# Performance work log

Hardware: AMD Instinct MI355X
Metric: run time of the kernel (lower is better)

The kernel has to match this reference:

```python
import jax, jax.numpy as jnp
import numpy as np

PADDING = 1
STRIDE = 1

def setup_inputs() -> dict:
    key = jax.random.key(0)
    k1, k2 = jax.random.split(key)
    x = jax.random.normal(k1, (32, 64, 64, 64), dtype=jnp.float32)
    # kaiming_normal fan_out, relu: std = sqrt(2 / (out_ch * k * k))
    fan_out = 128 * 3 * 3
    std = np.sqrt(2.0 / fan_out).astype(np.float32)
    weight = jax.random.normal(k2, (128, 64, 3, 3), dtype=jnp.float32) * std
    bias = jnp.zeros((128,), dtype=jnp.float32)
    return {"x": x, "weight": weight, "bias": bias}

def reference(x, weight, bias):
    # Faithful to the unfold+multiply+sum path, which computes a standard
    # cross-correlation conv2d (torch conv semantics) with stride/padding.
    out = jax.lax.conv_general_dilated(
        x, weight,
        window_strides=(STRIDE, STRIDE),
        padding=[(PADDING, PADDING), (PADDING, PADDING)],
        dimension_numbers=("NCHW", "OIHW", "NCHW"),
    )
    return out + bias[None, :, None, None]
```

## Files before the change

### kernel.cpp

```cpp
#include <hip/hip_runtime.h>


typedef short short8 __attribute__((ext_vector_type(8)));
typedef float f32x4  __attribute__((ext_vector_type(4)));

static __device__ __forceinline__ unsigned short f2bf(float f) {
    unsigned int u = __float_as_uint(f);
    u = (u + 0x7FFFu + ((u >> 16) & 1u)) >> 16;
    return (unsigned short)u;
}
static __device__ __forceinline__ unsigned int pk2(float lo, float hi) {
    return (unsigned int)f2bf(lo) | ((unsigned int)f2bf(hi) << 16);
}
static __device__ __forceinline__ void gload16(const void* g, void* l) {
    __builtin_amdgcn_global_load_lds(
        (const __attribute__((address_space(1))) void*)g,
        (__attribute__((address_space(3))) void*)l, 16, 0, 0);
}

__global__ __launch_bounds__(256)
void prep_xp(const float* __restrict__ x, unsigned short* __restrict__ xP)
{
    const int hp = blockIdx.x, n = blockIdx.y, tid = threadIdx.x;
    unsigned short* rowBase = xP + (((size_t)n * 66 + hp) * 66) * 64;
    if (hp == 0 || hp == 65) {
        uint4 z; z.x = z.y = z.z = z.w = 0u;
        for (int i = tid; i < 528; i += 256) ((uint4*)rowBase)[i] = z;
        return;
    }
    __shared__ float T[64][65];
    const int h = hp - 1;
    const size_t nbase = (size_t)n * 262144 + (size_t)h * 64;
    #pragma unroll
    for (int i = 0; i < 16; ++i) {
        int idx = tid + i * 256;
        int ci = idx >> 6, w = idx & 63;
        T[ci][w] = x[nbase + (size_t)ci * 4096 + w];
    }
    __syncthreads();
    if (tid < 16) {
        uint4 z; z.x = z.y = z.z = z.w = 0u;
        int wp = (tid >> 3) * 65;
        ((uint4*)(rowBase + wp * 64))[tid & 7] = z;
    }
    const int w = tid >> 2, cg = tid & 3;
    const int wp = w + 1;
    #pragma unroll
    for (int t = 0; t < 2; ++t) {
        const int g = cg * 2 + t;
        uint4 v;
        v.x = pk2(T[g*8+0][w], T[g*8+1][w]);
        v.y = pk2(T[g*8+2][w], T[g*8+3][w]);
        v.z = pk2(T[g*8+4][w], T[g*8+5][w]);
        v.w = pk2(T[g*8+6][w], T[g*8+7][w]);
        *(uint4*)(rowBase + wp * 64 + ((g ^ (wp & 7)) * 8)) = v;
    }
}

__global__ __launch_bounds__(256)
void prep_wS(const float* __restrict__ w, unsigned short* __restrict__ wS)
{
    int t = blockIdx.x * 256 + threadIdx.x;
    if (t >= 9216) return;
    int gp = t & 7, p = (t >> 3) % 9, co = (t >> 3) / 9;
    int g = gp ^ (co & 7);
    uint4 v;
    const float* src = w + (size_t)(co * 64 + g * 8) * 9 + p;
    v.x = pk2(src[0*9], src[1*9]);
    v.y = pk2(src[2*9], src[3*9]);
    v.z = pk2(src[4*9], src[5*9]);
    v.w = pk2(src[6*9], src[7*9]);
    *(uint4*)(wS + (size_t)t * 8) = v;
}

#define ABYTES 16384
#define BBYTES 16384
#define BUFBYTES (ABYTES + BBYTES)
#define TOTAL_LDS (2 * BUFBYTES)

__global__ __launch_bounds__(256, 3)
void conv_mfma8(const unsigned short* __restrict__ xP,
                const unsigned short* __restrict__ wS,
                const float* __restrict__ bias,
                float* __restrict__ out)
{
    extern __shared__ __align__(16) char lds[];

    const int tid  = threadIdx.x;
    const int bid  = blockIdx.x;
    const int swz  = (bid & 7) * 128 + (bid >> 3);
    const int n    = swz >> 5;
    const int h0   = (swz & 31) * 2;
    const int wid  = tid >> 6, lane = tid & 63;
    const int cb   = wid >> 1;
    const int sh   = wid & 1;
    const int l15  = lane & 15, l4 = lane >> 4;

    const char* aSrc = (const char*)wS +
        ((size_t)(wid * 32 + (lane >> 3)) * 1152 + (lane & 7) * 16);
    const char* bSrc = (const char*)xP +
        ((((size_t)n * 66 + h0 + (wid >> 1)) * 66 + (wid & 1) * 32 + (lane >> 3)) * 128 +
         (lane & 7) * 16);
    char* aDst = lds + wid * 4096;
    char* bDst = lds + ABYTES + wid * 4096;

    #pragma unroll
    for (int k = 0; k < 4; ++k) gload16(aSrc + k * 9216, aDst + k * 1024);
    #pragma unroll
    for (int k = 0; k < 4; ++k) gload16(bSrc + k * 1024, bDst + k * 1024);
    __syncthreads();

    f32x4 acc[4][4];
    #pragma unroll
    for (int mf = 0; mf < 4; ++mf)
        #pragma unroll
        for (int nf = 0; nf < 4; ++nf)
            acc[mf][nf] = (f32x4)0.0f;

    #pragma unroll
    for (int p = 0; p < 9; ++p) {
        const int kw = p % 3;
        if (p < 8) {
            const int pn  = p + 1;
            const int off = ((pn / 3) * 66 + (pn % 3)) * 128;
            char* aD = aDst + ((pn & 1) ? BUFBYTES : 0);
            char* bD = bDst + ((pn & 1) ? BUFBYTES : 0);
            #pragma unroll
            for (int k = 0; k < 4; ++k) gload16(aSrc + pn * 128 + k * 9216, aD + k * 1024);
            #pragma unroll
            for (int k = 0; k < 4; ++k) gload16(bSrc + off + k * 1024, bD + k * 1024);
        }

        const char* A = lds + ((p & 1) ? BUFBYTES : 0);
        const char* B = A + ABYTES;
        #pragma unroll
        for (int c = 0; c < 2; ++c) {
            short8 Af[4], Bf[4];
            #pragma unroll
            for (int mf = 0; mf < 4; ++mf) {
                const int co = cb * 64 + mf * 16 + l15;
                Af[mf] = *(const short8*)(A + co * 128 + (((c * 4 + l4) ^ (co & 7)) * 16));
            }
            #pragma unroll
            for (int nf = 0; nf < 4; ++nf) {
                const int sp = sh * 64 + nf * 16 + l15;
                Bf[nf] = *(const short8*)(B + sp * 128 + (((c * 4 + l4) ^ ((sp + kw) & 7)) * 16));
            }
            __builtin_amdgcn_s_setprio(1);
            #pragma unroll
            for (int mf = 0; mf < 4; ++mf)
                #pragma unroll
                for (int nf = 0; nf < 4; ++nf)
                    acc[mf][nf] = __builtin_amdgcn_mfma_f32_16x16x32_bf16(
                        Af[mf], Bf[nf], acc[mf][nf], 0, 0, 0);
            __builtin_amdgcn_s_setprio(0);
        }
        __syncthreads();
    }

    {
        const int h = h0 + sh;
        #pragma unroll
        for (int mf = 0; mf < 4; ++mf) {
            const f32x4 bv4 = *(const f32x4*)(bias + cb * 64 + mf * 16 + l4 * 4);
            #pragma unroll
            for (int r = 0; r < 4; ++r) {
                const int co = cb * 64 + mf * 16 + l4 * 4 + r;
                float* orow = out + (((size_t)n * 128 + co) * 64 + h) * 64;
                #pragma unroll
                for (int nf = 0; nf < 4; ++nf)
                    orow[nf * 16 + l15] = acc[mf][nf][r] + bv4[r];
            }
        }
    }
}

__global__ __launch_bounds__(256, 4)
void conv2d_f32_tiled(const float* __restrict__ x,
                      const float* __restrict__ wgt,
                      const float* __restrict__ bias,
                      float* __restrict__ out)
{
    __shared__ float Xlds[8][10][66];
    __shared__ float Wlds[32][72];
    const int tid = threadIdx.x;
    const int co0 = blockIdx.x * 32, h0 = blockIdx.y * 8, n = blockIdx.z;
    const int tco = tid >> 6, lane = tid & 63;
    float acc[8][8];
    #pragma unroll
    for (int i = 0; i < 8; ++i)
        #pragma unroll
        for (int j = 0; j < 8; ++j) acc[i][j] = 0.0f;
    for (int cc = 0; cc < 8; ++cc) {
        const int ci0 = cc * 8;
        for (int idx = tid; idx < 8 * 10 * 66; idx += 256) {
            const int ww = idx % 66, t = idx / 66, hh = t % 10, ci = t / 10;
            const int gh = h0 + hh - 1, gw = ww - 1;
            float v = 0.0f;
            if ((unsigned)gh < 64u && (unsigned)gw < 64u)
                v = x[(((size_t)n * 64 + ci0 + ci) * 64 + gh) * 64 + gw];
            Xlds[ci][hh][ww] = v;
        }
        for (int idx = tid; idx < 32 * 72; idx += 256) {
            const int r = idx % 72, co = idx / 72;
            Wlds[co][r] = wgt[(size_t)(co0 + co) * 576 + ci0 * 9 + r];
        }
        __syncthreads();
        for (int ci = 0; ci < 8; ++ci)
            #pragma unroll
            for (int kh = 0; kh < 3; ++kh)
                #pragma unroll
                for (int kw = 0; kw < 3; ++kw) {
                    float wv[8];
                    #pragma unroll
                    for (int i = 0; i < 8; ++i) wv[i] = Wlds[tco * 8 + i][ci * 9 + kh * 3 + kw];
                    #pragma unroll
                    for (int j = 0; j < 8; ++j) {
                        const float xv = Xlds[ci][j + kh][lane + kw];
                        #pragma unroll
                        for (int i = 0; i < 8; ++i) acc[i][j] = fmaf(wv[i], xv, acc[i][j]);
                    }
                }
        __syncthreads();
    }
    #pragma unroll
    for (int i = 0; i < 8; ++i) {
        const int co = co0 + tco * 8 + i;
        const float b = bias[co];
        #pragma unroll
        for (int j = 0; j < 8; ++j)
            out[(((size_t)n * 128 + co) * 64 + (h0 + j)) * 64 + lane] = acc[i][j] + b;
    }
}

extern "C" void kernel_launch(void* const* d_in, const int* in_sizes, int n_in,
                              void* d_out, int out_size, void* d_ws, size_t ws_size,
                              hipStream_t stream)
{
    const float* x    = (const float*)d_in[0];
    const float* wgt  = (const float*)d_in[1];
    const float* bias = (const float*)d_in[2];
    float* out        = (float*)d_out;

    const size_t XP_BYTES = (size_t)32 * 66 * 66 * 64 * 2;
    const size_t WS_BYTES = (size_t)128 * 9 * 64 * 2;

    if (ws_size < XP_BYTES + WS_BYTES) {
        dim3 grid(4, 8, 32);
        conv2d_f32_tiled<<<grid, 256, 0, stream>>>(x, wgt, bias, out);
        return;
    }

    unsigned short* xP = (unsigned short*)d_ws;
    unsigned short* wS = (unsigned short*)((char*)d_ws + XP_BYTES);

    (void)hipFuncSetAttribute((const void*)conv_mfma8,
                              hipFuncAttributeMaxDynamicSharedMemorySize, TOTAL_LDS);

    prep_xp<<<dim3(66, 32), 256, 0, stream>>>(x, xP);
    prep_wS<<<dim3(36), 256, 0, stream>>>(wgt, wS);
    conv_mfma8<<<dim3(1024), 256, TOTAL_LDS, stream>>>(xP, wS, bias, out);
}
```

Baseline: 44.15 us.

## Keep weights resident in LDS and stream input rows through a ring buffer

Replaces the 1024-block, per-tap double-buffered conv kernel with 256 blocks of 512 threads. Each block loads all 9 weight taps for 64 output channels into LDS once and keeps a 6-row ring of padded input rows. It then processes 16 output rows in four iterations, prefetching the next 4 input rows into registers while it computes. This is meant to remove the repeated per-tap global reloads of weights and overlapping input rows and to cut barrier count. The cost is about 121KB of LDS per block and a much smaller grid (256 blocks), which may leave CUs underused and expose load latency.

```diff
diff --git a/kernel.cpp b/kernel.cpp
--- a/kernel.cpp
+++ b/kernel.cpp
@@ -73,104 +73,136 @@
     *(uint4*)(wS + (size_t)t * 8) = v;
 }
 
-#define ABYTES 16384
-#define BBYTES 16384
-#define BUFBYTES (ABYTES + BBYTES)
-#define TOTAL_LDS (2 * BUFBYTES)
-
-__global__ __launch_bounds__(256, 3)
-void conv_mfma8(const unsigned short* __restrict__ xP,
+#define XROWB 8448
+#define WOFF  50688
+#define TOTAL_LDS (50688 + 73728)
+
+__global__ __launch_bounds__(512, 2)
+void conv_mfma9(const unsigned short* __restrict__ xP,
                 const unsigned short* __restrict__ wS,
                 const float* __restrict__ bias,
                 float* __restrict__ out)
 {
     extern __shared__ __align__(16) char lds[];
 
-    const int tid  = threadIdx.x;
-    const int bid  = blockIdx.x;
-    const int swz  = (bid & 7) * 128 + (bid >> 3);
-    const int n    = swz >> 5;
-    const int h0   = (swz & 31) * 2;
-    const int wid  = tid >> 6, lane = tid & 63;
-    const int cb   = wid >> 1;
-    const int sh   = wid & 1;
-    const int l15  = lane & 15, l4 = lane >> 4;
-
-    const char* aSrc = (const char*)wS +
-        ((size_t)(wid * 32 + (lane >> 3)) * 1152 + (lane & 7) * 16);
-    const char* bSrc = (const char*)xP +
-        ((((size_t)n * 66 + h0 + (wid >> 1)) * 66 + (wid & 1) * 32 + (lane >> 3)) * 128 +
-         (lane & 7) * 16);
-    char* aDst = lds + wid * 4096;
-    char* bDst = lds + ABYTES + wid * 4096;
-
-    #pragma unroll
-    for (int k = 0; k < 4; ++k) gload16(aSrc + k * 9216, aDst + k * 1024);
-    #pragma unroll
-    for (int k = 0; k < 4; ++k) gload16(bSrc + k * 1024, bDst + k * 1024);
+    const int tid = threadIdx.x;
+    const int bid = blockIdx.x;
+    const int n   = bid >> 3;
+    const int cb  = (bid >> 2) & 1;
+    const int hq  = bid & 3;
+    const int wid = tid >> 6, lane = tid & 63;
+    const int wm  = wid >> 2;
+    const int wn  = wid & 3;
+    const int l15 = lane & 15, l4 = lane >> 4;
+    const int widoff = wid * 1024;
+
+    const unsigned short* xPn = xP + (size_t)n * (66 * 66 * 64);
+    const int hbase = hq * 16;
+
+    #pragma unroll
+    for (int k = 0; k < 9; ++k) {
+        const int Gw = tid + k * 512;
+        const int slot = Gw & 7, col = (Gw >> 3) & 63, p = Gw >> 9;
+        gload16(wS + ((((size_t)(cb * 64 + col) * 9 + p) * 8 + slot) << 3),
+                lds + WOFF + k * 8192 + widoff);
+    }
+    #pragma unroll
+    for (int rr = 0; rr < 6; ++rr) {
+        const int hp = hbase + rr;
+        const int slot = hp % 6;
+        const unsigned short* srcRow = xPn + (size_t)hp * 4224;
+        gload16(srcRow + tid * 8, lds + slot * XROWB + widoff);
+        if (tid < 16)
+            gload16(srcRow + (512 + tid) * 8, lds + slot * XROWB + 8192);
+    }
     __syncthreads();
 
-    f32x4 acc[4][4];
-    #pragma unroll
-    for (int mf = 0; mf < 4; ++mf)
-        #pragma unroll
-        for (int nf = 0; nf < 4; ++nf)
-            acc[mf][nf] = (f32x4)0.0f;
-
-    #pragma unroll
-    for (int p = 0; p < 9; ++p) {
-        const int kw = p % 3;
-        if (p < 8) {
-            const int pn  = p + 1;
-            const int off = ((pn / 3) * 66 + (pn % 3)) * 128;
-            char* aD = aDst + ((pn & 1) ? BUFBYTES : 0);
-            char* bD = bDst + ((pn & 1) ? BUFBYTES : 0);
-            #pragma unroll
-            for (int k = 0; k < 4; ++k) gload16(aSrc + pn * 128 + k * 9216, aD + k * 1024);
-            #pragma unroll
-            for (int k = 0; k < 4; ++k) gload16(bSrc + off + k * 1024, bD + k * 1024);
-        }
-
-        const char* A = lds + ((p & 1) ? BUFBYTES : 0);
-        const char* B = A + ABYTES;
-        #pragma unroll
-        for (int c = 0; c < 2; ++c) {
-            short8 Af[4], Bf[4];
-            #pragma unroll
-            for (int mf = 0; mf < 4; ++mf) {
-                const int co = cb * 64 + mf * 16 + l15;
-                Af[mf] = *(const short8*)(A + co * 128 + (((c * 4 + l4) ^ (co & 7)) * 16));
-            }
-            #pragma unroll
-            for (int nf = 0; nf < 4; ++nf) {
-                const int sp = sh * 64 + nf * 16 + l15;
-                Bf[nf] = *(const short8*)(B + sp * 128 + (((c * 4 + l4) ^ ((sp + kw) & 7)) * 16));
-            }
-            __builtin_amdgcn_s_setprio(1);
-            #pragma unroll
-            for (int mf = 0; mf < 4; ++mf)
-                #pragma unroll
-                for (int nf = 0; nf < 4; ++nf)
-                    acc[mf][nf] = __builtin_amdgcn_mfma_f32_16x16x32_bf16(
-                        Af[mf], Bf[nf], acc[mf][nf], 0, 0, 0);
-            __builtin_amdgcn_s_setprio(0);
-        }
-        __syncthreads();
-    }
-
-    {
-        const int h = h0 + sh;
-        #pragma unroll
-        for (int mf = 0; mf < 4; ++mf) {
-            const f32x4 bv4 = *(const f32x4*)(bias + cb * 64 + mf * 16 + l4 * 4);
-            #pragma unroll
-            for (int r = 0; r < 4; ++r) {
-                const int co = cb * 64 + mf * 16 + l4 * 4 + r;
-                float* orow = out + (((size_t)n * 128 + co) * 64 + h) * 64;
-                #pragma unroll
-                for (int nf = 0; nf < 4; ++nf)
-                    orow[nf * 16 + l15] = acc[mf][nf][r] + bv4[r];
-            }
+    #pragma unroll
+    for (int it = 0; it < 4; ++it) {
+        const int h0 = hbase + it * 4;
+
+        uint4 xr[4]; uint4 xtail;
+        if (it < 3) {
+            #pragma unroll
+            for (int rr = 0; rr < 4; ++rr)
+                xr[rr] = *(const uint4*)(xPn + (size_t)(h0 + 6 + rr) * 4224 + tid * 8);
+            if (tid < 64)
+                xtail = *(const uint4*)(xPn + (size_t)(h0 + 6 + (tid >> 4)) * 4224 +
+                                        (512 + (tid & 15)) * 8);
+        }
+
+        f32x4 acc[2][4];
+        #pragma unroll
+        for (int mf = 0; mf < 2; ++mf)
+            #pragma unroll
+            for (int nf = 0; nf < 4; ++nf)
+                acc[mf][nf] = (f32x4)0.0f;
+
+        #pragma unroll
+        for (int p = 0; p < 9; ++p) {
+            const int kh = p / 3, kw = p - kh * 3;
+            const int rowslot = (h0 + wn + kh) % 6;
+            const char* xrow = lds + rowslot * XROWB;
+            const char* wpl  = lds + WOFF + p * 8192;
+            #pragma unroll
+            for (int c = 0; c < 2; ++c) {
+                short8 Af[2], Bf[4];
+                #pragma unroll
+                for (int mf = 0; mf < 2; ++mf) {
+                    const int col = wm * 32 + mf * 16 + l15;
+                    Af[mf] = *(const short8*)(wpl + col * 128 +
+                                              (((c * 4 + l4) ^ (col & 7)) * 16));
+                }
+                #pragma unroll
+                for (int nf = 0; nf < 4; ++nf) {
+                    const int wp = nf * 16 + l15 + kw;
+                    Bf[nf] = *(const short8*)(xrow + wp * 128 +
+                                              (((c * 4 + l4) ^ (wp & 7)) * 16));
+                }
+                __builtin_amdgcn_s_setprio(1);
+                #pragma unroll
+                for (int mf = 0; mf < 2; ++mf)
+                    #pragma unroll
+                    for (int nf = 0; nf < 4; ++nf)
+                        acc[mf][nf] = __builtin_amdgcn_mfma_f32_16x16x32_bf16(
+                            Af[mf], Bf[nf], acc[mf][nf], 0, 0, 0);
+                __builtin_amdgcn_s_setprio(0);
+            }
+        }
+
+        {
+            const int h = h0 + wn;
+            #pragma unroll
+            for (int mf = 0; mf < 2; ++mf) {
+                const f32x4 bv4 = *(const f32x4*)(bias + cb * 64 + wm * 32 + mf * 16 + l4 * 4);
+                #pragma unroll
+                for (int r = 0; r < 4; ++r) {
+                    const int co = cb * 64 + wm * 32 + mf * 16 + l4 * 4 + r;
+                    float* orow = out + (((size_t)n * 128 + co) * 64 + h) * 64;
+                    #pragma unroll
+                    for (int nf = 0; nf < 4; ++nf)
+                        orow[nf * 16 + l15] = acc[mf][nf][r] + bv4[r];
+                }
+            }
+        }
+
+        if (it < 3) {
+            __builtin_amdgcn_sched_barrier(0);
+            __builtin_amdgcn_s_barrier();
+            __builtin_amdgcn_sched_barrier(0);
+            #pragma unroll
+            for (int rr = 0; rr < 4; ++rr) {
+                const int slot = (h0 + 6 + rr) % 6;
+                *(uint4*)(lds + slot * XROWB + tid * 16) = xr[rr];
+            }
+            if (tid < 64) {
+                const int slot = (h0 + 6 + (tid >> 4)) % 6;
+                *(uint4*)(lds + slot * XROWB + (512 + (tid & 15)) * 16) = xtail;
+            }
+            __builtin_amdgcn_sched_barrier(0);
+            asm volatile("s_waitcnt lgkmcnt(0)" ::: "memory");
+            __builtin_amdgcn_s_barrier();
+            __builtin_amdgcn_sched_barrier(0);
         }
     }
 }
@@ -243,7 +275,7 @@
     float* out        = (float*)d_out;
 
     const size_t XP_BYTES = (size_t)32 * 66 * 66 * 64 * 2;
-    const size_t WS_BYTES = (size_t)128 * 9 * 64 * 2;
+    const size_t WS_BYTES = (size_t)9216 * 16;
 
     if (ws_size < XP_BYTES + WS_BYTES) {
         dim3 grid(4, 8, 32);
@@ -254,10 +286,10 @@
     unsigned short* xP = (unsigned short*)d_ws;
     unsigned short* wS = (unsigned short*)((char*)d_ws + XP_BYTES);
 
-    (void)hipFuncSetAttribute((const void*)conv_mfma8,
+    (void)hipFuncSetAttribute((const void*)conv_mfma9,
                               hipFuncAttributeMaxDynamicSharedMemorySize, TOTAL_LDS);
 
     prep_xp<<<dim3(66, 32), 256, 0, stream>>>(x, xP);
     prep_wS<<<dim3(36), 256, 0, stream>>>(wgt, wS);
-    conv_mfma8<<<dim3(1024), 256, TOTAL_LDS, stream>>>(xP, wS, bias, out);
-}
+    conv_mfma9<<<dim3(256), 512, TOTAL_LDS, stream>>>(xP, wS, bias, out);
+}
```

Measured after the change: 45.84 us. 3.8% more time.

## Stage a six-row input window in LDS once and stream weights per half-tap

Applied to the files above, without the earlier changes.

The conv kernel now uses 512-thread blocks that each compute four output rows. The six padded input rows they need are loaded into LDS once, and all nine taps read from that window by shifting offsets, instead of reloading an input tile for every tap. Weights are re-laid out into 18 half-channel chunks that are double-buffered through a small LDS area, one chunk per step. This cuts redundant global-to-LDS input traffic and halo reloads, at the cost of about 66KB of LDS per block, which may limit occupancy, and a barrier on each of the 18 steps.

```diff
diff --git a/kernel.cpp b/kernel.cpp
--- a/kernel.cpp
+++ b/kernel.cpp
@@ -58,56 +58,53 @@
 }
 
 __global__ __launch_bounds__(256)
-void prep_wS(const float* __restrict__ w, unsigned short* __restrict__ wS)
-{
-    int t = blockIdx.x * 256 + threadIdx.x;
-    if (t >= 9216) return;
-    int gp = t & 7, p = (t >> 3) % 9, co = (t >> 3) / 9;
-    int g = gp ^ (co & 7);
+void prep_wS2(const float* __restrict__ w, unsigned short* __restrict__ wS)
+{
+    int u = blockIdx.x * 256 + threadIdx.x;
+    if (u >= 9216) return;
+    int slot = u & 3, co = (u >> 2) & 127, s = u >> 9;
+    int p = s >> 1, ch = s & 1;
+    int g = slot ^ (co & 3);
+    const float* src = w + (size_t)(co * 64 + ch * 32 + g * 8) * 9 + p;
     uint4 v;
-    const float* src = w + (size_t)(co * 64 + g * 8) * 9 + p;
     v.x = pk2(src[0*9], src[1*9]);
     v.y = pk2(src[2*9], src[3*9]);
     v.z = pk2(src[4*9], src[5*9]);
     v.w = pk2(src[6*9], src[7*9]);
-    *(uint4*)(wS + (size_t)t * 8) = v;
-}
-
-#define ABYTES 16384
-#define BBYTES 16384
-#define BUFBYTES (ABYTES + BBYTES)
-#define TOTAL_LDS (2 * BUFBYTES)
-
-__global__ __launch_bounds__(256, 3)
-void conv_mfma8(const unsigned short* __restrict__ xP,
-                const unsigned short* __restrict__ wS,
-                const float* __restrict__ bias,
-                float* __restrict__ out)
+    *(uint4*)(wS + (size_t)u * 8) = v;
+}
+
+#define XWIN  50688
+#define WHALF 8192
+#define TOTAL_LDS (XWIN + 2*WHALF)
+
+__global__ __launch_bounds__(512, 4)
+void conv_mfma11(const unsigned short* __restrict__ xP,
+                 const unsigned short* __restrict__ wS,
+                 const float* __restrict__ bias,
+                 float* __restrict__ out)
 {
     extern __shared__ __align__(16) char lds[];
+    char* wb = lds + XWIN;
 
     const int tid  = threadIdx.x;
-    const int bid  = blockIdx.x;
-    const int swz  = (bid & 7) * 128 + (bid >> 3);
-    const int n    = swz >> 5;
-    const int h0   = (swz & 31) * 2;
+    const int hq   = blockIdx.x;
+    const int n    = blockIdx.y;
+    const int h0   = hq * 4;
     const int wid  = tid >> 6, lane = tid & 63;
-    const int cb   = wid >> 1;
-    const int sh   = wid & 1;
+    const int cb   = wid >> 2;
+    const int wrow = wid & 3;
     const int l15  = lane & 15, l4 = lane >> 4;
 
-    const char* aSrc = (const char*)wS +
-        ((size_t)(wid * 32 + (lane >> 3)) * 1152 + (lane & 7) * 16);
-    const char* bSrc = (const char*)xP +
-        ((((size_t)n * 66 + h0 + (wid >> 1)) * 66 + (wid & 1) * 32 + (lane >> 3)) * 128 +
-         (lane & 7) * 16);
-    char* aDst = lds + wid * 4096;
-    char* bDst = lds + ABYTES + wid * 4096;
-
-    #pragma unroll
-    for (int k = 0; k < 4; ++k) gload16(aSrc + k * 9216, aDst + k * 1024);
-    #pragma unroll
-    for (int k = 0; k < 4; ++k) gload16(bSrc + k * 1024, bDst + k * 1024);
+    const unsigned short* xPn = xP + (size_t)n * (66 * 66 * 64);
+    const char* wSb = (const char*)wS;
+
+    #pragma unroll
+    for (int rr = 0; rr < 6; ++rr)
+        gload16(xPn + (size_t)(h0 + rr) * 4224 + tid * 8, lds + rr * 8448 + tid * 16);
+    if (lane < 16 && wid < 6)
+        gload16(xPn + (size_t)(h0 + wid) * 4224 + (512 + lane) * 8, lds + wid * 8448 + 8192);
+    gload16(wSb + tid * 16, wb + tid * 16);
     __syncthreads();
 
     f32x4 acc[4][4];
@@ -118,48 +115,37 @@
             acc[mf][nf] = (f32x4)0.0f;
 
     #pragma unroll
-    for (int p = 0; p < 9; ++p) {
-        const int kw = p % 3;
-        if (p < 8) {
-            const int pn  = p + 1;
-            const int off = ((pn / 3) * 66 + (pn % 3)) * 128;
-            char* aD = aDst + ((pn & 1) ? BUFBYTES : 0);
-            char* bD = bDst + ((pn & 1) ? BUFBYTES : 0);
+    for (int s = 0; s < 18; ++s) {
+        const int p  = s >> 1;
+        const int ch = s & 1;
+        const int kh = p / 3, kw = p - kh * 3;
+
+        if (s < 17)
+            gload16(wSb + ((s + 1) * 512 + tid) * 16, wb + ((s + 1) & 1) * WHALF + tid * 16);
+
+        const char* wcur = wb + (s & 1) * WHALF;
+        const char* xrow = lds + (wrow + kh) * 8448;
+
+        short8 Bf[4];
+        #pragma unroll
+        for (int nf = 0; nf < 4; ++nf) {
+            const int wp = nf * 16 + l15 + kw;
+            Bf[nf] = *(const short8*)(xrow + wp * 128 + (((ch * 4 + l4) ^ (wp & 7)) * 16));
+        }
+        #pragma unroll
+        for (int mf = 0; mf < 4; ++mf) {
+            const int co = cb * 64 + mf * 16 + l15;
+            short8 Af = *(const short8*)(wcur + co * 64 + ((l4 ^ (co & 3)) * 16));
             #pragma unroll
-            for (int k = 0; k < 4; ++k) gload16(aSrc + pn * 128 + k * 9216, aD + k * 1024);
-            #pragma unroll
-            for (int k = 0; k < 4; ++k) gload16(bSrc + off + k * 1024, bD + k * 1024);
-        }
-
-        const char* A = lds + ((p & 1) ? BUFBYTES : 0);
-        const char* B = A + ABYTES;
-        #pragma unroll
-        for (int c = 0; c < 2; ++c) {
-            short8 Af[4], Bf[4];
-            #pragma unroll
-            for (int mf = 0; mf < 4; ++mf) {
-                const int co = cb * 64 + mf * 16 + l15;
-                Af[mf] = *(const short8*)(A + co * 128 + (((c * 4 + l4) ^ (co & 7)) * 16));
-            }
-            #pragma unroll
-            for (int nf = 0; nf < 4; ++nf) {
-                const int sp = sh * 64 + nf * 16 + l15;
-                Bf[nf] = *(const short8*)(B + sp * 128 + (((c * 4 + l4) ^ ((sp + kw) & 7)) * 16));
-            }
-            __builtin_amdgcn_s_setprio(1);
-            #pragma unroll
-            for (int mf = 0; mf < 4; ++mf)
-                #pragma unroll
-                for (int nf = 0; nf < 4; ++nf)
-                    acc[mf][nf] = __builtin_amdgcn_mfma_f32_16x16x32_bf16(
-                        Af[mf], Bf[nf], acc[mf][nf], 0, 0, 0);
-            __builtin_amdgcn_s_setprio(0);
-        }
-        __syncthreads();
+            for (int nf = 0; nf < 4; ++nf)
+                acc[mf][nf] = __builtin_amdgcn_mfma_f32_16x16x32_bf16(
+                    Af, Bf[nf], acc[mf][nf], 0, 0, 0);
+        }
+        if (s < 17) __syncthreads();
     }
 
     {
-        const int h = h0 + sh;
+        const int h = h0 + wrow;
         #pragma unroll
         for (int mf = 0; mf < 4; ++mf) {
             const f32x4 bv4 = *(const f32x4*)(bias + cb * 64 + mf * 16 + l4 * 4);
@@ -243,7 +229,7 @@
     float* out        = (float*)d_out;
 
     const size_t XP_BYTES = (size_t)32 * 66 * 66 * 64 * 2;
-    const size_t WS_BYTES = (size_t)128 * 9 * 64 * 2;
+    const size_t WS_BYTES = (size_t)9216 * 16;
 
     if (ws_size < XP_BYTES + WS_BYTES) {
         dim3 grid(4, 8, 32);
@@ -254,10 +240,10 @@
     unsigned short* xP = (unsigned short*)d_ws;
     unsigned short* wS = (unsigned short*)((char*)d_ws + XP_BYTES);
 
-    (void)hipFuncSetAttribute((const void*)conv_mfma8,
+    (void)hipFuncSetAttribute((const void*)conv_mfma11,
                               hipFuncAttributeMaxDynamicSharedMemorySize, TOTAL_LDS);
 
     prep_xp<<<dim3(66, 32), 256, 0, stream>>>(x, xP);
-    prep_wS<<<dim3(36), 256, 0, stream>>>(wgt, wS);
-    conv_mfma8<<<dim3(1024), 256, TOTAL_LDS, stream>>>(xP, wS, bias, out);
-}
+    prep_wS2<<<dim3(36), 256, 0, stream>>>(wgt, wS);
+    conv_mfma11<<<dim3(16, 32), 512, TOTAL_LDS, stream>>>(xP, wS, bias, out);
+}
```

New measurement: 45.95 us. +4.1%, slower.
